# Kernel optimization log

Hardware: AMD Instinct MI355X
Metric: run time of the kernel (lower is better)

## Reference

```python
import jax, jax.numpy as jnp
import numpy as np

B, S, D, H = 4, 2048, 1024, 16
HD = D // H  # head size = 64


def setup_inputs() -> dict:
    key = jax.random.key(0)
    ks = jax.random.split(key, 5)
    x = jax.random.normal(ks[0], (B, S, D), dtype=jnp.float32)
    scale = 1.0 / np.sqrt(D)
    Wq = jax.random.normal(ks[1], (H, D, HD), dtype=jnp.float32) * scale
    Wk = jax.random.normal(ks[2], (H, D, HD), dtype=jnp.float32) * scale
    Wv = jax.random.normal(ks[3], (H, D, HD), dtype=jnp.float32) * scale
    W_O = jax.random.normal(ks[4], (D, D), dtype=jnp.float32) * scale
    return {"x": x, "Wq": Wq, "Wk": Wk, "Wv": Wv, "W_O": W_O}


def reference(x, Wq, Wk, Wv, W_O):
    # Per-head Q/K/V projections, batched across heads via einsum.
    q = jnp.einsum("bsd,hde->bhse", x, Wq)  # [B,H,S,HD]
    k = jnp.einsum("bsd,hde->bhse", x, Wk)
    v = jnp.einsum("bsd,hde->bhse", x, Wv)
    scores = jnp.einsum("bhse,bhte->bhst", q, k) / jnp.sqrt(
        jnp.asarray(HD, dtype=x.dtype)
    )  # [B,H,S,S]
    # Causal mask (GPT-style attention head).
    causal = jnp.tril(jnp.ones((S, S), dtype=bool))
    scores = jnp.where(causal, scores, jnp.finfo(scores.dtype).min)
    attn = jax.nn.softmax(scores, axis=-1)
    out = jnp.einsum("bhst,bhte->bhse", attn, v)  # [B,H,S,HD]
    # Concat heads: [B,S,H,HD] -> [B,S,D]
    concat = out.transpose(0, 2, 1, 3).reshape(B, S, D)
    # nn.Linear(D, D, bias=False): y = x @ W_O^T
    return concat @ W_O.T
```

## Files before the change

kernel.cpp:

```cpp
#include <hip/hip_runtime.h>
#include <hip/hip_bf16.h>

#define BB 4
#define SS 2048
#define DD 1024
#define HH 16
#define HDD 64

typedef __attribute__((ext_vector_type(8))) short bf16x8;
typedef __attribute__((ext_vector_type(8))) unsigned short u16x8;
typedef __attribute__((ext_vector_type(4))) float f32x4;
typedef __attribute__((ext_vector_type(4))) unsigned int u32x4;

#define GLD_LDS16(g, l) \
    __builtin_amdgcn_global_load_lds((const __attribute__((address_space(1))) void*)(g), \
                                     (__attribute__((address_space(3))) void*)(l), 16, 0, 0)

__device__ __forceinline__ unsigned short f32_to_bf16(float f) {
    unsigned int u = __float_as_uint(f);
    u += 0x7fffu + ((u >> 16) & 1u);
    return (unsigned short)(u >> 16);
}

__device__ __forceinline__ unsigned int cvt_pk_bf16(float lo, float hi) {
    unsigned int r;
    asm("v_cvt_pk_bf16_f32 %0, %1, %2" : "=v"(r) : "v"(lo), "v"(hi));
    return r;
}

__device__ __forceinline__ float fmax3(float a, float b, float c) {
    return fmaxf(fmaxf(a, b), c);
}

__global__ __launch_bounds__(256) void convert_f32_bf16(
    const float* __restrict__ in, unsigned short* __restrict__ out, int n4) {
    int stride = gridDim.x * blockDim.x;
    for (int i = blockIdx.x * blockDim.x + threadIdx.x; i < n4; i += stride) {
        float4 v = ((const float4*)in)[i];
        ushort4 o;
        o.x = f32_to_bf16(v.x); o.y = f32_to_bf16(v.y);
        o.z = f32_to_bf16(v.z); o.w = f32_to_bf16(v.w);
        ((ushort4*)out)[i] = o;
    }
}

__global__ __launch_bounds__(256) void pack_wqkv(
    const float* __restrict__ Wq, const float* __restrict__ Wk,
    const float* __restrict__ Wv, unsigned short* __restrict__ WT) {
    int bid = blockIdx.x;
    int w = bid >> 8, h = (bid >> 4) & 15, db = bid & 15;
    const float* src = (w == 0) ? Wq : ((w == 1) ? Wk : Wv);
    __shared__ float tile[64][68];
    int t = threadIdx.x;
    for (int p = t; p < 1024; p += 256) {
        int row = p >> 4, c4 = p & 15;
        float4 v = *(const float4*)(src + ((size_t)(h * 1024 + db * 64 + row)) * 64 + c4 * 4);
        tile[row][c4 * 4 + 0] = v.x; tile[row][c4 * 4 + 1] = v.y;
        tile[row][c4 * 4 + 2] = v.z; tile[row][c4 * 4 + 3] = v.w;
    }
    __syncthreads();
    size_t wbase = (size_t)w * 1024 * 1024;
    for (int p = t; p < 512; p += 256) {
        int e = p >> 3, c = p & 7;
        u16x8 pk;
#pragma unroll
        for (int j = 0; j < 8; ++j) pk[j] = f32_to_bf16(tile[c * 8 + j][e]);
        *(u16x8*)(WT + wbase + (size_t)(h * 64 + e) * 1024 + db * 64 + c * 8) = pk;
    }
}

template <int EPI>
__global__ __launch_bounds__(256) void gemm128(
    const unsigned short* __restrict__ A, const unsigned short* __restrict__ Bm,
    void* __restrict__ C0, void* __restrict__ C1, void* __restrict__ C2, int NBt) {
    __shared__ unsigned short As[128 * 64];
    __shared__ unsigned short Bs[128 * 64];
    int cpx = gridDim.x >> 3;
    int bid = (blockIdx.x & 7) * cpx + (blockIdx.x >> 3);
    int mb = bid / NBt, nb = bid % NBt;
    int tid = threadIdx.x;
    int lane = tid & 63, wid = tid >> 6;
    int wm = wid >> 1, wn = wid & 1;
    int g = lane >> 4, lr = lane & 15;
    int srow = lane >> 3, sch = lane & 7;
    int scol = (sch ^ srow) * 8;
    const int M0 = mb * 128, N0 = nb * 128;

    f32x4 acc[4][4] = {};

    for (int kt = 0; kt < 16; ++kt) {
        __syncthreads();
#pragma unroll
        for (int i = 0; i < 4; ++i) {
            int c = wid * 4 + i;
            int row = c * 8 + srow;
            GLD_LDS16(A + (size_t)(M0 + row) * 1024 + kt * 64 + scol, As + c * 512);
            GLD_LDS16(Bm + (size_t)(N0 + row) * 1024 + kt * 64 + scol, Bs + c * 512);
        }
        __syncthreads();
#pragma unroll
        for (int kk = 0; kk < 2; ++kk) {
            bf16x8 af[4], bfr[4];
#pragma unroll
            for (int i = 0; i < 4; ++i) {
                int row = wm * 64 + i * 16 + lr;
                int ch = (kk * 4 + g) ^ (row & 7);
                af[i] = *(const bf16x8*)(As + row * 64 + ch * 8);
                int rowb = wn * 64 + i * 16 + lr;
                int chb = (kk * 4 + g) ^ (rowb & 7);
                bfr[i] = *(const bf16x8*)(Bs + rowb * 64 + chb * 8);
            }
            __builtin_amdgcn_s_setprio(1);
#pragma unroll
            for (int i = 0; i < 4; ++i)
#pragma unroll
                for (int j = 0; j < 4; ++j)
                    acc[i][j] = __builtin_amdgcn_mfma_f32_16x16x32_bf16(af[i], bfr[j], acc[i][j], 0, 0, 0);
            __builtin_amdgcn_s_setprio(0);
        }
    }

    if constexpr (EPI == 0) {
        unsigned short* Qo = (unsigned short*)C0;
        unsigned short* Ko = (unsigned short*)C1;
        unsigned short* Vo = (unsigned short*)C2;
        const float QSCALE = 0.125f * 1.4426950408889634f;
#pragma unroll
        for (int i = 0; i < 4; ++i)
#pragma unroll
            for (int j = 0; j < 4; ++j)
#pragma unroll
                for (int r = 0; r < 4; ++r) {
                    int m = M0 + wm * 64 + i * 16 + g * 4 + r;
                    int n = N0 + wn * 64 + j * 16 + lr;
                    int b = m >> 11, s = m & 2047;
                    int w = n >> 10, h = (n >> 6) & 15, e = n & 63;
                    unsigned short* dst = (w == 0) ? Qo : ((w == 1) ? Ko : Vo);
                    float scl = (w == 0) ? QSCALE : 1.0f;
                    dst[((size_t)(b * HH + h) * SS + s) * HDD + e] = f32_to_bf16(acc[i][j][r] * scl);
                }
    } else {
        float* Co = (float*)C0;
#pragma unroll
        for (int i = 0; i < 4; ++i)
#pragma unroll
            for (int j = 0; j < 4; ++j)
#pragma unroll
                for (int r = 0; r < 4; ++r) {
                    int m = M0 + wm * 64 + i * 16 + g * 4 + r;
                    int n = N0 + wn * 64 + j * 16 + lr;
                    Co[(size_t)m * 1024 + n] = acc[i][j][r];
                }
    }
}

__global__ __launch_bounds__(256) void transpose_v(
    const unsigned short* __restrict__ V, unsigned short* __restrict__ VT) {
    int bh = blockIdx.x >> 5, sb = blockIdx.x & 31;
    __shared__ unsigned short tile[64][72];
    const unsigned short* src = V + ((size_t)bh * SS + sb * 64) * HDD;
    int t = threadIdx.x;
    for (int p = t; p < 512; p += 256) {
        int row = p >> 3, c = p & 7;
        *(u16x8*)&tile[row][c * 8] = *(const u16x8*)(src + row * 64 + c * 8);
    }
    __syncthreads();
    unsigned short* dst = VT + (size_t)bh * HDD * SS + sb * 64;
    for (int p = t; p < 512; p += 256) {
        int e = p >> 3, c = p & 7;
        u16x8 pk;
#pragma unroll
        for (int j = 0; j < 8; ++j) pk[j] = tile[c * 8 + j][e];
        *(u16x8*)(dst + (size_t)e * SS + c * 8) = pk;
    }
}

__global__ __launch_bounds__(256, 4) void attn_fwd(
    const unsigned short* __restrict__ Q, const unsigned short* __restrict__ K,
    const unsigned short* __restrict__ VT, unsigned short* __restrict__ O) {
    int bid = blockIdx.x;
    int qb = 15 - (bid >> 6);
    int bh = bid & 63;
    int b = bh >> 4, h = bh & 15;
    int tid = threadIdx.x, lane = tid & 63, w = tid >> 6;
    int g = lane >> 4, lr = lane & 15;
    int srow = lane >> 3, sch = lane & 7;
    int scol = (sch ^ srow) * 8;

    __shared__ unsigned short smem[16384];

    const int q0 = qb * 128;
    const unsigned short* Qp = Q + ((size_t)bh * SS + q0 + w * 32) * HDD;
    const unsigned short* Kp = K + (size_t)bh * SS * HDD;
    const unsigned short* Vp = VT + (size_t)bh * HDD * SS;

    bf16x8 qf[2][2];
#pragma unroll
    for (int qg = 0; qg < 2; ++qg) {
        qf[qg][0] = *(const bf16x8*)(Qp + (qg * 16 + lr) * 64 + g * 8);
        qf[qg][1] = *(const bf16x8*)(Qp + (qg * 16 + lr) * 64 + 32 + g * 8);
    }

    float m_[2] = {-3.0e38f, -3.0e38f};
    float l_[2] = {0.f, 0.f};
    f32x4 acc[2][4] = {};

    const int nt = 2 * qb + 2;

#pragma unroll
    for (int i = 0; i < 2; ++i) {
        int c = w * 2 + i;
        int row = c * 8 + srow;
        GLD_LDS16(Kp + (size_t)row * HDD + scol, smem + c * 512);
        GLD_LDS16(Vp + (size_t)row * SS + scol, smem + 8192 + c * 512);
    }
    __syncthreads();

    for (int it = 0; it < nt; ++it) {
        unsigned short* Kcur = smem + (it & 1) * 4096;
        unsigned short* Vcur = smem + 8192 + (it & 1) * 4096;
        if (it + 1 < nt) {
            int t1 = (it + 1) * 64;
            unsigned short* Knxt = smem + ((it & 1) ^ 1) * 4096;
            unsigned short* Vnxt = smem + 8192 + ((it & 1) ^ 1) * 4096;
#pragma unroll
            for (int i = 0; i < 2; ++i) {
                int c = w * 2 + i;
                int row = c * 8 + srow;
                GLD_LDS16(Kp + (size_t)(t1 + row) * HDD + scol, Knxt + c * 512);
                GLD_LDS16(Vp + (size_t)row * SS + t1 + scol, Vnxt + c * 512);
            }
        }
        int t0 = it * 64;

        f32x4 sacc[2][4] = {};
        __builtin_amdgcn_s_setprio(1);
#pragma unroll
        for (int kk = 0; kk < 2; ++kk)
#pragma unroll
            for (int ct = 0; ct < 4; ++ct) {
                int row = ct * 16 + lr;
                int ch = (kk * 4 + g) ^ (row & 7);
                bf16x8 kf = *(const bf16x8*)(Kcur + row * 64 + ch * 8);
#pragma unroll
                for (int qg = 0; qg < 2; ++qg)
                    sacc[qg][ct] = __builtin_amdgcn_mfma_f32_16x16x32_bf16(kf, qf[qg][kk], sacc[qg][ct], 0, 0, 0);
            }
        __builtin_amdgcn_s_setprio(0);

        if (it >= nt - 2) {
#pragma unroll
            for (int qg = 0; qg < 2; ++qg) {
                int kmax = q0 + w * 32 + qg * 16 + lr - t0;
#pragma unroll
                for (int ct = 0; ct < 4; ++ct)
#pragma unroll
                    for (int r = 0; r < 4; ++r)
                        if (ct * 16 + g * 4 + r > kmax) sacc[qg][ct][r] = -3.0e38f;
            }
        }

        bf16x8 pvf[2][2];
#pragma unroll
        for (int qg = 0; qg < 2; ++qg) {
            float t = fmax3(
                fmax3(fmax3(sacc[qg][0][0], sacc[qg][0][1], sacc[qg][0][2]),
                      fmax3(sacc[qg][0][3], sacc[qg][1][0], sacc[qg][1][1]),
                      fmax3(sacc[qg][1][2], sacc[qg][1][3], sacc[qg][2][0])),
                fmax3(sacc[qg][2][1], sacc[qg][2][2], sacc[qg][2][3]),
                fmax3(sacc[qg][3][0], sacc[qg][3][1],
                      fmaxf(sacc[qg][3][2], sacc[qg][3][3])));
            t = fmaxf(t, __shfl_xor(t, 16));
            t = fmaxf(t, __shfl_xor(t, 32));
            bool need = t > m_[qg] + 8.0f;
            if (__any((int)need)) {
                float nm = fmaxf(m_[qg], t);
                float sf = exp2f(m_[qg] - nm);
                m_[qg] = nm;
                l_[qg] *= sf;
#pragma unroll
                for (int ct = 0; ct < 4; ++ct)
#pragma unroll
                    for (int r = 0; r < 4; ++r) acc[qg][ct][r] *= sf;
            }
            float rs0 = 0.f, rs1 = 0.f, rs2 = 0.f, rs3 = 0.f;
#pragma unroll
            for (int ct = 0; ct < 4; ++ct) {
                float p0 = exp2f(sacc[qg][ct][0] - m_[qg]);
                float p1 = exp2f(sacc[qg][ct][1] - m_[qg]);
                float p2 = exp2f(sacc[qg][ct][2] - m_[qg]);
                float p3 = exp2f(sacc[qg][ct][3] - m_[qg]);
                sacc[qg][ct][0] = p0; sacc[qg][ct][1] = p1;
                sacc[qg][ct][2] = p2; sacc[qg][ct][3] = p3;
                rs0 += p0; rs1 += p1; rs2 += p2; rs3 += p3;
            }
            float rs = (rs0 + rs1) + (rs2 + rs3);
            rs += __shfl_xor(rs, 16);
            rs += __shfl_xor(rs, 32);
            l_[qg] += rs;

            unsigned int pk[4][2];
#pragma unroll
            for (int ct = 0; ct < 4; ++ct) {
                pk[ct][0] = cvt_pk_bf16(sacc[qg][ct][0], sacc[qg][ct][1]);
                pk[ct][1] = cvt_pk_bf16(sacc[qg][ct][2], sacc[qg][ct][3]);
            }
            unsigned int out[2][4];
#pragma unroll
            for (int s5 = 0; s5 < 2; ++s5)
#pragma unroll
                for (int s1 = 0; s1 < 2; ++s1) {
                    unsigned int a = pk[2 * s5][s1];
                    unsigned int bq = pk[2 * s5 + 1][s1];
                    asm("v_permlane32_swap_b32 %0, %1" : "+v"(a), "+v"(bq));
                    asm("v_permlane16_swap_b32 %0, %1" : "+v"(a), "+v"(bq));
                    out[s5][s1] = a;
                    out[s5][2 + s1] = bq;
                }
#pragma unroll
            for (int kk2 = 0; kk2 < 2; ++kk2) {
                u32x4 tmp;
                tmp[0] = out[kk2][0]; tmp[1] = out[kk2][1];
                tmp[2] = out[kk2][2]; tmp[3] = out[kk2][3];
                pvf[qg][kk2] = __builtin_bit_cast(bf16x8, tmp);
            }
        }

#pragma unroll
        for (int kk2 = 0; kk2 < 2; ++kk2)
#pragma unroll
            for (int ct2 = 0; ct2 < 4; ++ct2) {
                int row = ct2 * 16 + lr;
                int ch = (kk2 * 4 + g) ^ (row & 7);
                bf16x8 vf = *(const bf16x8*)(Vcur + row * 64 + ch * 8);
                __builtin_amdgcn_s_setprio(1);
#pragma unroll
                for (int qg = 0; qg < 2; ++qg)
                    acc[qg][ct2] = __builtin_amdgcn_mfma_f32_16x16x32_bf16(vf, pvf[qg][kk2], acc[qg][ct2], 0, 0, 0);
                __builtin_amdgcn_s_setprio(0);
            }

        __syncthreads();
    }

#pragma unroll
    for (int qg = 0; qg < 2; ++qg) {
        float invl = 1.0f / l_[qg];
#pragma unroll
        for (int ct2 = 0; ct2 < 4; ++ct2)
#pragma unroll
            for (int r = 0; r < 4; ++r)
                smem[(w * 32 + qg * 16 + lr) * 72 + ct2 * 16 + g * 4 + r] =
                    f32_to_bf16(acc[qg][ct2][r] * invl);
    }
    __syncthreads();
#pragma unroll
    for (int itr = 0; itr < 4; ++itr) {
        int idx = itr * 256 + tid;
        int row = idx >> 3, seg = idx & 7;
        u16x8 vv = *(const u16x8*)&smem[row * 72 + seg * 8];
        *(u16x8*)(O + ((size_t)(b * SS + q0 + row)) * DD + h * 64 + seg * 8) = vv;
    }
}

extern "C" void kernel_launch(void* const* d_in, const int* in_sizes, int n_in,
                              void* d_out, int out_size, void* d_ws, size_t ws_size,
                              hipStream_t stream) {
    (void)in_sizes; (void)n_in; (void)out_size; (void)ws_size;
    const float* x  = (const float*)d_in[0];
    const float* Wq = (const float*)d_in[1];
    const float* Wk = (const float*)d_in[2];
    const float* Wv = (const float*)d_in[3];
    const float* WO = (const float*)d_in[4];
    float* out = (float*)d_out;

    char* ws = (char*)d_ws;
    unsigned short* xb    = (unsigned short*)(ws + 0);
    unsigned short* wqkvT = (unsigned short*)(ws + 16777216);
    unsigned short* wob   = (unsigned short*)(ws + 23068672);
    unsigned short* Qb    = (unsigned short*)(ws + 25165824);
    unsigned short* Kb    = (unsigned short*)(ws + 41943040);
    unsigned short* Vb    = (unsigned short*)(ws + 58720256);
    unsigned short* VTb   = (unsigned short*)(ws + 75497472);
    unsigned short* Ob    = (unsigned short*)(ws + 92274688);

    convert_f32_bf16<<<2048, 256, 0, stream>>>(x, xb, (BB * SS * DD) / 4);
    convert_f32_bf16<<<1024, 256, 0, stream>>>(WO, wob, (DD * DD) / 4);
    pack_wqkv<<<768, 256, 0, stream>>>(Wq, Wk, Wv, wqkvT);
    gemm128<0><<<64 * 24, 256, 0, stream>>>(xb, wqkvT, (void*)Qb, (void*)Kb, (void*)Vb, 24);
    transpose_v<<<2048, 256, 0, stream>>>(Vb, VTb);
    attn_fwd<<<1024, 256, 0, stream>>>(Qb, Kb, VTb, Ob);
    gemm128<1><<<64 * 8, 256, 0, stream>>>(Ob, wob, (void*)out, nullptr, nullptr, 8);
}
```

Before: 177.7 us.

## Use 256x128 GEMM tiles with double-buffered LDS prefetch interleaved with MFMA

Replaces the 128x128 single-buffered GEMM with a 256x128 tile run by 512 threads (8 waves), with A/B staged in two LDS buffers. The next K-slice is loaded with global_load_lds while the current slice is multiplied, and one barrier per iteration replaces two. This is meant to hide global load latency and cut per-tile B traffic, at the cost of more LDS (96KB per block), fewer blocks, and higher register pressure under launch_bounds(512,2).

Result: slower. 192.3 us (+8.2%).

```diff
diff --git a/kernel.cpp b/kernel.cpp
--- a/kernel.cpp
+++ b/kernel.cpp
@@ -70,11 +70,11 @@
 }
 
 template <int EPI>
-__global__ __launch_bounds__(256) void gemm128(
+__global__ __launch_bounds__(512, 2) void gemm256(
     const unsigned short* __restrict__ A, const unsigned short* __restrict__ Bm,
     void* __restrict__ C0, void* __restrict__ C1, void* __restrict__ C2, int NBt) {
-    __shared__ unsigned short As[128 * 64];
-    __shared__ unsigned short Bs[128 * 64];
+    __shared__ unsigned short As[2][256 * 64];
+    __shared__ unsigned short Bs[2][128 * 64];
     int cpx = gridDim.x >> 3;
     int bid = (blockIdx.x & 7) * cpx + (blockIdx.x >> 3);
     int mb = bid / NBt, nb = bid % NBt;
@@ -84,38 +84,63 @@
     int g = lane >> 4, lr = lane & 15;
     int srow = lane >> 3, sch = lane & 7;
     int scol = (sch ^ srow) * 8;
-    const int M0 = mb * 128, N0 = nb * 128;
+    const int M0 = mb * 256, N0 = nb * 128;
 
     f32x4 acc[4][4] = {};
 
+#pragma unroll
+    for (int l = 0; l < 4; ++l) {
+        int c = wid * 4 + l;
+        GLD_LDS16(A + (size_t)(M0 + c * 8 + srow) * 1024 + scol, &As[0][c * 512]);
+    }
+#pragma unroll
+    for (int l = 0; l < 2; ++l) {
+        int c = wid * 2 + l;
+        GLD_LDS16(Bm + (size_t)(N0 + c * 8 + srow) * 1024 + scol, &Bs[0][c * 512]);
+    }
+
     for (int kt = 0; kt < 16; ++kt) {
-        __syncthreads();
-#pragma unroll
-        for (int i = 0; i < 4; ++i) {
-            int c = wid * 4 + i;
-            int row = c * 8 + srow;
-            GLD_LDS16(A + (size_t)(M0 + row) * 1024 + kt * 64 + scol, As + c * 512);
-            GLD_LDS16(Bm + (size_t)(N0 + row) * 1024 + kt * 64 + scol, Bs + c * 512);
-        }
-        __syncthreads();
-#pragma unroll
-        for (int kk = 0; kk < 2; ++kk) {
-            bf16x8 af[4], bfr[4];
+        int cur = kt & 1;
+        asm volatile("s_waitcnt vmcnt(0)" ::: "memory");
+        __builtin_amdgcn_s_barrier();
+
+        bf16x8 af[2][4];
+#pragma unroll
+        for (int kk = 0; kk < 2; ++kk)
 #pragma unroll
             for (int i = 0; i < 4; ++i) {
                 int row = wm * 64 + i * 16 + lr;
                 int ch = (kk * 4 + g) ^ (row & 7);
-                af[i] = *(const bf16x8*)(As + row * 64 + ch * 8);
-                int rowb = wn * 64 + i * 16 + lr;
+                af[kk][i] = *(const bf16x8*)&As[cur][row * 64 + ch * 8];
+            }
+
+        bool st = (kt + 1 < 16);
+        int kc1 = (kt + 1) * 64;
+#pragma unroll
+        for (int q = 0; q < 4; ++q) {
+            bf16x8 bfr[2];
+            int rowb = wn * 64 + q * 16 + lr;
+#pragma unroll
+            for (int kk = 0; kk < 2; ++kk) {
                 int chb = (kk * 4 + g) ^ (rowb & 7);
-                bfr[i] = *(const bf16x8*)(Bs + rowb * 64 + chb * 8);
+                bfr[kk] = *(const bf16x8*)&Bs[cur][rowb * 64 + chb * 8];
+            }
+            if (st) {
+                int ca = wid * 4 + q;
+                GLD_LDS16(A + (size_t)(M0 + ca * 8 + srow) * 1024 + kc1 + scol,
+                          &As[cur ^ 1][ca * 512]);
+                if (q < 2) {
+                    int cb = wid * 2 + q;
+                    GLD_LDS16(Bm + (size_t)(N0 + cb * 8 + srow) * 1024 + kc1 + scol,
+                              &Bs[cur ^ 1][cb * 512]);
+                }
             }
             __builtin_amdgcn_s_setprio(1);
 #pragma unroll
-            for (int i = 0; i < 4; ++i)
-#pragma unroll
-                for (int j = 0; j < 4; ++j)
-                    acc[i][j] = __builtin_amdgcn_mfma_f32_16x16x32_bf16(af[i], bfr[j], acc[i][j], 0, 0, 0);
+            for (int kk = 0; kk < 2; ++kk)
+#pragma unroll
+                for (int i = 0; i < 4; ++i)
+                    acc[i][q] = __builtin_amdgcn_mfma_f32_16x16x32_bf16(af[kk][i], bfr[kk], acc[i][q], 0, 0, 0);
             __builtin_amdgcn_s_setprio(0);
         }
     }
@@ -128,28 +153,28 @@
 #pragma unroll
         for (int i = 0; i < 4; ++i)
 #pragma unroll
-            for (int j = 0; j < 4; ++j)
+            for (int q = 0; q < 4; ++q)
 #pragma unroll
                 for (int r = 0; r < 4; ++r) {
                     int m = M0 + wm * 64 + i * 16 + g * 4 + r;
-                    int n = N0 + wn * 64 + j * 16 + lr;
+                    int n = N0 + wn * 64 + q * 16 + lr;
                     int b = m >> 11, s = m & 2047;
                     int w = n >> 10, h = (n >> 6) & 15, e = n & 63;
                     unsigned short* dst = (w == 0) ? Qo : ((w == 1) ? Ko : Vo);
                     float scl = (w == 0) ? QSCALE : 1.0f;
-                    dst[((size_t)(b * HH + h) * SS + s) * HDD + e] = f32_to_bf16(acc[i][j][r] * scl);
+                    dst[((size_t)(b * HH + h) * SS + s) * HDD + e] = f32_to_bf16(acc[i][q][r] * scl);
                 }
     } else {
         float* Co = (float*)C0;
 #pragma unroll
         for (int i = 0; i < 4; ++i)
 #pragma unroll
-            for (int j = 0; j < 4; ++j)
+            for (int q = 0; q < 4; ++q)
 #pragma unroll
                 for (int r = 0; r < 4; ++r) {
                     int m = M0 + wm * 64 + i * 16 + g * 4 + r;
-                    int n = N0 + wn * 64 + j * 16 + lr;
-                    Co[(size_t)m * 1024 + n] = acc[i][j][r];
+                    int n = N0 + wn * 64 + q * 16 + lr;
+                    Co[(size_t)m * 1024 + n] = acc[i][q][r];
                 }
     }
 }
@@ -387,8 +412,8 @@
     convert_f32_bf16<<<2048, 256, 0, stream>>>(x, xb, (BB * SS * DD) / 4);
     convert_f32_bf16<<<1024, 256, 0, stream>>>(WO, wob, (DD * DD) / 4);
     pack_wqkv<<<768, 256, 0, stream>>>(Wq, Wk, Wv, wqkvT);
-    gemm128<0><<<64 * 24, 256, 0, stream>>>(xb, wqkvT, (void*)Qb, (void*)Kb, (void*)Vb, 24);
+    gemm256<0><<<32 * 24, 512, 0, stream>>>(xb, wqkvT, (void*)Qb, (void*)Kb, (void*)Vb, 24);
     transpose_v<<<2048, 256, 0, stream>>>(Vb, VTb);
     attn_fwd<<<1024, 256, 0, stream>>>(Qb, Kb, VTb, Ob);
-    gemm128<1><<<64 * 8, 256, 0, stream>>>(Ob, wob, (void*)out, nullptr, nullptr, 8);
-}
+    gemm256<1><<<32 * 8, 512, 0, stream>>>(Ob, wob, (void*)out, nullptr, nullptr, 8);
+}
```

## Fuse V transpose into QKV GEMM epilogue via LDS-staged transposed stores

Applied to the files above, without the earlier changes.

The QKV projection GEMM now writes V directly in transposed [B,H,HD,S] layout. For V column blocks it stages the accumulator tile through LDS with an XOR swizzle and then issues coalesced 16-byte stores. This removes the separate transpose_v kernel launch and its extra 16MB read/write round trip through global memory. The cost is an extra LDS pass and two barriers in the epilogue of one third of the GEMM blocks. The Q/K branch also skips the per-element destination selection.

Result: no change. 175.1 us (-1.5%).

```diff
diff --git a/kernel.cpp b/kernel.cpp
--- a/kernel.cpp
+++ b/kernel.cpp
@@ -73,8 +73,7 @@
 __global__ __launch_bounds__(256) void gemm128(
     const unsigned short* __restrict__ A, const unsigned short* __restrict__ Bm,
     void* __restrict__ C0, void* __restrict__ C1, void* __restrict__ C2, int NBt) {
-    __shared__ unsigned short As[128 * 64];
-    __shared__ unsigned short Bs[128 * 64];
+    __shared__ unsigned short sh[2][128 * 64];
     int cpx = gridDim.x >> 3;
     int bid = (blockIdx.x & 7) * cpx + (blockIdx.x >> 3);
     int mb = bid / NBt, nb = bid % NBt;
@@ -94,8 +93,8 @@
         for (int i = 0; i < 4; ++i) {
             int c = wid * 4 + i;
             int row = c * 8 + srow;
-            GLD_LDS16(A + (size_t)(M0 + row) * 1024 + kt * 64 + scol, As + c * 512);
-            GLD_LDS16(Bm + (size_t)(N0 + row) * 1024 + kt * 64 + scol, Bs + c * 512);
+            GLD_LDS16(A + (size_t)(M0 + row) * 1024 + kt * 64 + scol, &sh[0][c * 512]);
+            GLD_LDS16(Bm + (size_t)(N0 + row) * 1024 + kt * 64 + scol, &sh[1][c * 512]);
         }
         __syncthreads();
 #pragma unroll
@@ -105,10 +104,10 @@
             for (int i = 0; i < 4; ++i) {
                 int row = wm * 64 + i * 16 + lr;
                 int ch = (kk * 4 + g) ^ (row & 7);
-                af[i] = *(const bf16x8*)(As + row * 64 + ch * 8);
+                af[i] = *(const bf16x8*)&sh[0][row * 64 + ch * 8];
                 int rowb = wn * 64 + i * 16 + lr;
                 int chb = (kk * 4 + g) ^ (rowb & 7);
-                bfr[i] = *(const bf16x8*)(Bs + rowb * 64 + chb * 8);
+                bfr[i] = *(const bf16x8*)&sh[1][rowb * 64 + chb * 8];
             }
             __builtin_amdgcn_s_setprio(1);
 #pragma unroll
@@ -121,24 +120,51 @@
     }
 
     if constexpr (EPI == 0) {
-        unsigned short* Qo = (unsigned short*)C0;
-        unsigned short* Ko = (unsigned short*)C1;
-        unsigned short* Vo = (unsigned short*)C2;
-        const float QSCALE = 0.125f * 1.4426950408889634f;
-#pragma unroll
-        for (int i = 0; i < 4; ++i)
-#pragma unroll
-            for (int j = 0; j < 4; ++j)
-#pragma unroll
-                for (int r = 0; r < 4; ++r) {
-                    int m = M0 + wm * 64 + i * 16 + g * 4 + r;
-                    int n = N0 + wn * 64 + j * 16 + lr;
-                    int b = m >> 11, s = m & 2047;
-                    int w = n >> 10, h = (n >> 6) & 15, e = n & 63;
-                    unsigned short* dst = (w == 0) ? Qo : ((w == 1) ? Ko : Vo);
-                    float scl = (w == 0) ? QSCALE : 1.0f;
-                    dst[((size_t)(b * HH + h) * SS + s) * HDD + e] = f32_to_bf16(acc[i][j][r] * scl);
-                }
+        if (nb < 16) {
+            unsigned short* Qo = (unsigned short*)C0;
+            unsigned short* Ko = (unsigned short*)C1;
+            const float QSCALE = 0.125f * 1.4426950408889634f;
+            unsigned short* dst = (nb < 8) ? Qo : Ko;
+            float scl = (nb < 8) ? QSCALE : 1.0f;
+#pragma unroll
+            for (int i = 0; i < 4; ++i)
+#pragma unroll
+                for (int j = 0; j < 4; ++j)
+#pragma unroll
+                    for (int r = 0; r < 4; ++r) {
+                        int m = M0 + wm * 64 + i * 16 + g * 4 + r;
+                        int n = N0 + wn * 64 + j * 16 + lr;
+                        int b = m >> 11, s = m & 2047;
+                        int h = (n >> 6) & 15, e = n & 63;
+                        dst[((size_t)(b * HH + h) * SS + s) * HDD + e] = f32_to_bf16(acc[i][j][r] * scl);
+                    }
+        } else {
+            unsigned short (*T)[128] = (unsigned short(*)[128])sh;
+            __syncthreads();
+#pragma unroll
+            for (int i = 0; i < 4; ++i)
+#pragma unroll
+                for (int j = 0; j < 4; ++j)
+#pragma unroll
+                    for (int r = 0; r < 4; ++r) {
+                        int nl = wn * 64 + j * 16 + lr;
+                        int ml = wm * 64 + i * 16 + g * 4 + r;
+                        T[nl][ml ^ ((nl & 7) << 3)] = f32_to_bf16(acc[i][j][r]);
+                    }
+            __syncthreads();
+            unsigned short* Vo = (unsigned short*)C2;
+            int b = M0 >> 11, s0 = M0 & 2047;
+            int nb16 = nb - 16;
+#pragma unroll
+            for (int itr = 0; itr < 8; ++itr) {
+                int idx = itr * 256 + tid;
+                int row = idx >> 4, seg = idx & 15;
+                u16x8 vv = *(const u16x8*)&T[row][(seg * 8) ^ ((row & 7) << 3)];
+                int h = (nb16 * 128 + row) >> 6;
+                int e = row & 63;
+                *(u16x8*)(Vo + (((size_t)(b * HH + h)) * HDD + e) * SS + s0 + seg * 8) = vv;
+            }
+        }
     } else {
         float* Co = (float*)C0;
 #pragma unroll
@@ -151,27 +177,6 @@
                     int n = N0 + wn * 64 + j * 16 + lr;
                     Co[(size_t)m * 1024 + n] = acc[i][j][r];
                 }
-    }
-}
-
-__global__ __launch_bounds__(256) void transpose_v(
-    const unsigned short* __restrict__ V, unsigned short* __restrict__ VT) {
-    int bh = blockIdx.x >> 5, sb = blockIdx.x & 31;
-    __shared__ unsigned short tile[64][72];
-    const unsigned short* src = V + ((size_t)bh * SS + sb * 64) * HDD;
-    int t = threadIdx.x;
-    for (int p = t; p < 512; p += 256) {
-        int row = p >> 3, c = p & 7;
-        *(u16x8*)&tile[row][c * 8] = *(const u16x8*)(src + row * 64 + c * 8);
-    }
-    __syncthreads();
-    unsigned short* dst = VT + (size_t)bh * HDD * SS + sb * 64;
-    for (int p = t; p < 512; p += 256) {
-        int e = p >> 3, c = p & 7;
-        u16x8 pk;
-#pragma unroll
-        for (int j = 0; j < 8; ++j) pk[j] = tile[c * 8 + j][e];
-        *(u16x8*)(dst + (size_t)e * SS + c * 8) = pk;
     }
 }
 
@@ -380,15 +385,13 @@
     unsigned short* wob   = (unsigned short*)(ws + 23068672);
     unsigned short* Qb    = (unsigned short*)(ws + 25165824);
     unsigned short* Kb    = (unsigned short*)(ws + 41943040);
-    unsigned short* Vb    = (unsigned short*)(ws + 58720256);
     unsigned short* VTb   = (unsigned short*)(ws + 75497472);
     unsigned short* Ob    = (unsigned short*)(ws + 92274688);
 
     convert_f32_bf16<<<2048, 256, 0, stream>>>(x, xb, (BB * SS * DD) / 4);
     convert_f32_bf16<<<1024, 256, 0, stream>>>(WO, wob, (DD * DD) / 4);
     pack_wqkv<<<768, 256, 0, stream>>>(Wq, Wk, Wv, wqkvT);
-    gemm128<0><<<64 * 24, 256, 0, stream>>>(xb, wqkvT, (void*)Qb, (void*)Kb, (void*)Vb, 24);
-    transpose_v<<<2048, 256, 0, stream>>>(Vb, VTb);
+    gemm128<0><<<64 * 24, 256, 0, stream>>>(xb, wqkvT, (void*)Qb, (void*)Kb, (void*)VTb, 24);
     attn_fwd<<<1024, 256, 0, stream>>>(Qb, Kb, VTb, Ob);
     gemm128<1><<<64 * 8, 256, 0, stream>>>(Ob, wob, (void*)out, nullptr, nullptr, 8);
 }
```
